# Kernel optimization log

Hardware: AMD Instinct MI355X
Metric: run time of the kernel (lower is better)

## Reference

```python
import jax, jax.numpy as jnp
import numpy as np

B, S, E, H = 4, 2048, 1024, 16
D = E // H  # head_dim = 64


def setup_inputs() -> dict:
    key = jax.random.key(0)
    ks = jax.random.split(key, 5)
    return {
        "x": jax.random.normal(ks[0], (B, S, E), dtype=jnp.float32),
        "w_qkv": jax.random.normal(ks[1], (3 * E, E), dtype=jnp.float32) * (E ** -0.5),
        "b_qkv": jax.random.normal(ks[2], (3 * E,), dtype=jnp.float32) * 0.02,
        "w_proj": jax.random.normal(ks[3], (E, E), dtype=jnp.float32) * (E ** -0.5),
        "b_proj": jax.random.normal(ks[4], (E,), dtype=jnp.float32) * 0.02,
    }


def reference(x, w_qkv, b_qkv, w_proj, b_proj):
    # fused QKV projection: [B,S,E] -> [B,S,3E] -> [B,S,3,H,D]
    qkv = (jnp.einsum("bse,fe->bsf", x, w_qkv) + b_qkv).reshape(B, S, 3, H, D)
    q, k, v = qkv[:, :, 0], qkv[:, :, 1], qkv[:, :, 2]  # each [B,S,H,D]
    scale = 1.0 / jnp.sqrt(jnp.asarray(D, dtype=q.dtype))
    scores = jnp.einsum("bqhd,bkhd->bhqk", q, k) * scale  # [B,H,S,S]
    attn = jax.nn.softmax(scores, axis=-1)
    out = jnp.einsum("bhqk,bkhd->bqhd", attn, v).reshape(B, S, E)
    return jnp.einsum("bse,fe->bsf", out, w_proj) + b_proj
```

## Files before the change

### kernel.cpp

```cpp
#include <hip/hip_runtime.h>
#include <cstdint>
#include <cstddef>

#define B_ 4
#define S_ 2048
#define E_ 1024
#define H_ 16
#define D_ 64
#define M_ (B_*S_)
#define NE_ ((size_t)B_*H_*S_*D_)

typedef unsigned int  u32;
typedef unsigned short u16;
typedef __attribute__((ext_vector_type(8))) short bf16x8;
typedef __attribute__((ext_vector_type(4))) float f32x4;
typedef __attribute__((ext_vector_type(2))) unsigned int u32x2;

__device__ __forceinline__ u16 f2bf(float x) {
    u32 u = __float_as_uint(x);
    u32 r = (u + 0x7FFFu + ((u >> 16) & 1u)) >> 16;
    return (u16)r;
}
__device__ __forceinline__ float bf2f(u16 h) { return __uint_as_float((u32)h << 16); }

__device__ __forceinline__ u32 cvtpk_bf16(float lo, float hi) {
    u32 r;
    asm("v_cvt_pk_bf16_f32 %0, %1, %2" : "=v"(r) : "v"(lo), "v"(hi));
    return r;
}

__device__ __forceinline__ void gload_lds16(const void* gsrc, void* lds) {
    __builtin_amdgcn_global_load_lds(
        (const __attribute__((address_space(1))) u32*)gsrc,
        (__attribute__((address_space(3))) u32*)lds, 16, 0, 0);
}


__global__ __launch_bounds__(256)
void convert_img(const float* __restrict__ src, u16* __restrict__ dh, u16* __restrict__ dl)
{
    const int tile = blockIdx.x;
    const int rt = tile >> 5, kt = tile & 31;
    const size_t tb = (size_t)tile * 2048;
    const int ci = threadIdx.x;
    const int l  = ci >> 3;
    const int ph = ci & 7;
    const int s  = ph ^ (l & 7);
    const int r  = (l << 1) | (s >> 2);
    const int k0 = (s & 3) << 3;
    const float* sp = src + ((size_t)(rt * 64 + r)) * 1024 + kt * 32 + k0;
    const float4 f0 = *(const float4*)sp;
    const float4 f1 = *(const float4*)(sp + 4);
    const float vals[8] = {f0.x, f0.y, f0.z, f0.w, f1.x, f1.y, f1.z, f1.w};
    __align__(16) short hs[8];
    __align__(16) short ls[8];
    #pragma unroll
    for (int j = 0; j < 8; ++j) {
        const u16 h = f2bf(vals[j]);
        hs[j] = (short)h;
        ls[j] = (short)f2bf(vals[j] - bf2f(h));
    }
    *(bf16x8*)(dh + tb + ci * 8) = *(const bf16x8*)hs;
    *(bf16x8*)(dl + tb + ci * 8) = *(const bf16x8*)ls;
}

template<int MODE>
__global__ __launch_bounds__(512, 2)
void gemm_mfma(const u16* __restrict__ AIh, const u16* __restrict__ AIl,
               const u16* __restrict__ BIh, const u16* __restrict__ BIl,
               const float* __restrict__ bias, float* __restrict__ Cout,
               u16* __restrict__ qh, u16* __restrict__ ql,
               u16* __restrict__ kh,
               u16* __restrict__ vh, u16* __restrict__ vl)
{
    __shared__ __align__(16) u16 sT[2][12][2048];

    const int tid = threadIdx.x, lane = tid & 63, w = tid >> 6;
    const int quad = lane >> 4, l15 = lane & 15;
    const int m0  = blockIdx.x * 256;
    const int n0  = blockIdx.y * 128;
    const int mt0 = blockIdx.x * 4;
    const int nt0 = blockIdx.y * 2;
    const int rw  = w >> 1;
    const int cw  = w & 1;

    const u16* srcq[6];
    #pragma unroll
    for (int it = 0; it < 6; ++it) {
        const int g = w * 6 + it;
        const int t = g >> 2, qtr = g & 3;
        const u16* img = (t < 4) ? AIh : (t < 8) ? AIl : (t < 10) ? BIh : BIl;
        const int rtile = (t < 8) ? (mt0 + (t & 3)) : (nt0 + (t & 1));
        srcq[it] = img + (size_t)rtile * (32 * 2048) + qtr * 512 + lane * 8;
    }

    f32x4 acc[4][4];
    #pragma unroll
    for (int i = 0; i < 4; ++i)
        #pragma unroll
        for (int j = 0; j < 4; ++j)
            acc[i][j] = (f32x4){0.f, 0.f, 0.f, 0.f};

    #pragma unroll
    for (int it = 0; it < 6; ++it)
        gload_lds16(srcq[it], (char*)&sT[0][0][0] + (w * 6 + it) * 1024);
    __syncthreads();

    #pragma unroll 2
    for (int kt = 0; kt < 32; ++kt) {
        const int cur = kt & 1;
        bf16x8 aH[4], aL[4], bH[4], bL[4];
        #pragma unroll
        for (int i = 0; i < 4; ++i) {
            const int r = i * 16 + l15, l = r >> 1;
            const int off = l * 64 + (((((r & 1) << 2) + quad) ^ (l & 7)) << 3);
            aH[i] = *(const bf16x8*)&sT[cur][rw][off];
            aL[i] = *(const bf16x8*)&sT[cur][4 + rw][off];
        }
        #pragma unroll
        for (int j = 0; j < 4; ++j) {
            const int r = j * 16 + l15, l = r >> 1;
            const int off = l * 64 + (((((r & 1) << 2) + quad) ^ (l & 7)) << 3);
            bH[j] = *(const bf16x8*)&sT[cur][8 + cw][off];
            bL[j] = *(const bf16x8*)&sT[cur][10 + cw][off];
        }
        if (kt < 31) {
            #pragma unroll
            for (int it = 0; it < 6; ++it)
                gload_lds16(srcq[it] + (size_t)(kt + 1) * 2048,
                            (char*)&sT[cur ^ 1][0][0] + (w * 6 + it) * 1024);
        }
        __builtin_amdgcn_s_setprio(1);
        #pragma unroll
        for (int i = 0; i < 4; ++i)
            #pragma unroll
            for (int j = 0; j < 4; ++j) {
                acc[i][j] = __builtin_amdgcn_mfma_f32_16x16x32_bf16(aL[i], bH[j], acc[i][j], 0, 0, 0);
                acc[i][j] = __builtin_amdgcn_mfma_f32_16x16x32_bf16(aH[i], bL[j], acc[i][j], 0, 0, 0);
                acc[i][j] = __builtin_amdgcn_mfma_f32_16x16x32_bf16(aH[i], bH[j], acc[i][j], 0, 0, 0);
            }
        __builtin_amdgcn_s_setprio(0);
        __syncthreads();
    }

    const int fbase = n0 + cw * 64;
    float bj[4];
    #pragma unroll
    for (int j = 0; j < 4; ++j) bj[j] = bias[fbase + j * 16 + l15];

    if (MODE == 0) {
        const int cR = fbase >> 10;
        const int hh = (fbase >> 6) & 15;
        #pragma unroll
        for (int i = 0; i < 4; ++i)
            #pragma unroll
            for (int j = 0; j < 4; ++j)
                #pragma unroll
                for (int reg = 0; reg < 4; ++reg) {
                    float val = acc[i][j][reg] + bj[j];
                    const int m = m0 + rw * 64 + i * 16 + quad * 4 + reg;
                    const int d = j * 16 + l15;
                    const int bb = m >> 11, s = m & 2047;
                    const int bh = bb * 16 + hh;
                    if (cR == 0) val *= 0.18033688011112042f;
                    const u16 h = f2bf(val);
                    if (cR == 0) {
                        const u16 lo = f2bf(val - bf2f(h));
                        const size_t idx = ((size_t)bh * 2048 + s) * 64 + d;
                        qh[idx] = h; ql[idx] = lo;
                    } else if (cR == 1) {
                        const size_t tile = (size_t)bh * 32 + (s >> 6);
                        const int r = s & 63;
                        const size_t off = (tile << 12) + r * 64 + (((d >> 3) ^ (r & 7)) << 3) + (d & 7);
                        kh[off] = h;
                    } else {
                        const u16 lo = f2bf(val - bf2f(h));
                        const size_t tile = (size_t)bh * 32 + (s >> 6);
                        const size_t off = (tile << 12) + d * 64 + ((((s & 63) >> 3) ^ (d & 7)) << 3) + (s & 7);
                        vh[off] = h; vl[off] = lo;
                    }
                }
    } else {
        #pragma unroll
        for (int i = 0; i < 4; ++i)
            #pragma unroll
            for (int j = 0; j < 4; ++j)
                #pragma unroll
                for (int reg = 0; reg < 4; ++reg) {
                    const int m = m0 + rw * 64 + i * 16 + quad * 4 + reg;
                    const int f = fbase + j * 16 + l15;
                    Cout[(size_t)m * 1024 + f] = acc[i][j][reg] + bj[j];
                }
    }
}

__global__ __launch_bounds__(256, 3)
void attn_mfma(const u16* __restrict__ qh, const u16* __restrict__ ql,
               const u16* __restrict__ kh,
               const u16* __restrict__ vh, const u16* __restrict__ vl,
               u16* __restrict__ oh, u16* __restrict__ ol)
{
    __shared__ __align__(16) u16 KV[3][4096];

    const int tid  = threadIdx.x;
    const int lane = tid & 63, w = tid >> 6;
    const int quad = lane >> 4, l15 = lane & 15;
    const int bh = blockIdx.y;
    const int q0 = blockIdx.x * 128 + w * 32;

    bf16x8 Qf[2][2][2];
    #pragma unroll
    for (int qs = 0; qs < 2; ++qs)
        #pragma unroll
        for (int kk = 0; kk < 2; ++kk) {
            const size_t idx = ((size_t)bh * S_ + q0 + qs * 16 + l15) * 64 + kk * 32 + quad * 8;
            Qf[qs][kk][0] = *(const bf16x8*)(qh + idx);
            Qf[qs][kk][1] = *(const bf16x8*)(ql + idx);
        }

    f32x4 O[2][4];
    float l_part[2] = {0.f, 0.f};
    #pragma unroll
    for (int qs = 0; qs < 2; ++qs)
        #pragma unroll
        for (int ds = 0; ds < 4; ++ds)
            O[qs][ds] = (f32x4){0.f, 0.f, 0.f, 0.f};

    const char* gk[3] = {(const char*)kh, (const char*)vh, (const char*)vl};

    for (int kt = 0; kt < S_ / 64; ++kt) {
        __syncthreads();
        const size_t tb = (((size_t)bh * 32 + kt) << 13);
        #pragma unroll
        for (int a = 0; a < 3; ++a)
            #pragma unroll
            for (int it = 0; it < 2; ++it) {
                const int off = w * 2048 + it * 1024;
                gload_lds16(gk[a] + tb + off + lane * 16, (char*)&KV[a][0] + off);
            }
        __syncthreads();

        f32x4 S[2][4];
        #pragma unroll
        for (int qs = 0; qs < 2; ++qs)
            #pragma unroll
            for (int ks = 0; ks < 4; ++ks)
                S[qs][ks] = (f32x4){-23.083120654223414f, -23.083120654223414f,
                                    -23.083120654223414f, -23.083120654223414f};

        __builtin_amdgcn_s_setprio(1);
        #pragma unroll
        for (int ks = 0; ks < 4; ++ks) {
            const int r = ks * 16 + l15;
            #pragma unroll
            for (int kk = 0; kk < 2; ++kk) {
                const int c = (kk * 4 + quad) ^ (r & 7);
                const bf16x8 Kh = *(const bf16x8*)&KV[0][r * 64 + c * 8];
                #pragma unroll
                for (int qs = 0; qs < 2; ++qs) {
                    S[qs][ks] = __builtin_amdgcn_mfma_f32_16x16x32_bf16(Kh, Qf[qs][kk][1], S[qs][ks], 0, 0, 0);
                    S[qs][ks] = __builtin_amdgcn_mfma_f32_16x16x32_bf16(Kh, Qf[qs][kk][0], S[qs][ks], 0, 0, 0);
                }
            }
        }
        __builtin_amdgcn_s_setprio(0);

        u32 PA[2][2][4];
        #pragma unroll
        for (int qs = 0; qs < 2; ++qs) {
            float lsum = 0.f;
            u32 PK[4][2];
            #pragma unroll
            for (int ks = 0; ks < 4; ++ks) {
                const float p0 = __builtin_exp2f(S[qs][ks][0]);
                const float p1 = __builtin_exp2f(S[qs][ks][1]);
                const float p2 = __builtin_exp2f(S[qs][ks][2]);
                const float p3 = __builtin_exp2f(S[qs][ks][3]);
                lsum += (p0 + p1) + (p2 + p3);
                PK[ks][0] = cvtpk_bf16(p0, p1);
                PK[ks][1] = cvtpk_bf16(p2, p3);
            }
            l_part[qs] += lsum;
            #pragma unroll
            for (int kk = 0; kk < 2; ++kk) {
                const u32x2 t0 = __builtin_amdgcn_permlane32_swap(PK[2 * kk][0], PK[2 * kk + 1][0], false, false);
                const u32x2 w02 = __builtin_amdgcn_permlane16_swap(t0.x, t0.y, false, false);
                const u32x2 t1 = __builtin_amdgcn_permlane32_swap(PK[2 * kk][1], PK[2 * kk + 1][1], false, false);
                const u32x2 w13 = __builtin_amdgcn_permlane16_swap(t1.x, t1.y, false, false);
                PA[qs][kk][0] = w02.x;
                PA[qs][kk][1] = w13.x;
                PA[qs][kk][2] = w02.y;
                PA[qs][kk][3] = w13.y;
            }
        }

        __builtin_amdgcn_s_setprio(1);
        #pragma unroll
        for (int kk = 0; kk < 2; ++kk) {
            union { u32 w4[4]; bf16x8 v; } pu0, pu1;
            #pragma unroll
            for (int c = 0; c < 4; ++c) { pu0.w4[c] = PA[0][kk][c]; pu1.w4[c] = PA[1][kk][c]; }
            const bf16x8 paf[2] = {pu0.v, pu1.v};
            #pragma unroll
            for (int ds = 0; ds < 4; ++ds) {
                const int r = ds * 16 + l15;
                const int c = (kk * 4 + quad) ^ (r & 7);
                const bf16x8 Vh = *(const bf16x8*)&KV[1][r * 64 + c * 8];
                const bf16x8 Vl = *(const bf16x8*)&KV[2][r * 64 + c * 8];
                #pragma unroll
                for (int qs = 0; qs < 2; ++qs) {
                    O[qs][ds] = __builtin_amdgcn_mfma_f32_16x16x32_bf16(Vl, paf[qs], O[qs][ds], 0, 0, 0);
                    O[qs][ds] = __builtin_amdgcn_mfma_f32_16x16x32_bf16(Vh, paf[qs], O[qs][ds], 0, 0, 0);
                }
            }
        }
        __builtin_amdgcn_s_setprio(0);
    }

    float linv[2];
    #pragma unroll
    for (int qs = 0; qs < 2; ++qs) {
        float rs = l_part[qs];
        rs += __shfl_xor(rs, 16);
        rs += __shfl_xor(rs, 32);
        linv[qs] = 1.f / rs;
    }

    const int bb = bh >> 4, hh = bh & 15;
    #pragma unroll
    for (int qs = 0; qs < 2; ++qs) {
        const float inv = linv[qs];
        const int s = q0 + qs * 16 + l15;
        const int m = bb * 2048 + s;
        const int mt = m >> 6, r = m & 63;
        const int l = r >> 1;
        const size_t tb0 = ((size_t)(mt * 32 + hh * 2)) * 2048;
        #pragma unroll
        for (int ds = 0; ds < 4; ++ds) {
            const int d0 = ds * 16 + quad * 4;
            const float v0 = O[qs][ds][0] * inv;
            const float v1 = O[qs][ds][1] * inv;
            const float v2 = O[qs][ds][2] * inv;
            const float v3 = O[qs][ds][3] * inv;
            const u32 h01 = cvtpk_bf16(v0, v1);
            const u32 h23 = cvtpk_bf16(v2, v3);
            const float r0 = v0 - bf2f((u16)h01);
            const float r1 = v1 - bf2f((u16)(h01 >> 16));
            const float r2 = v2 - bf2f((u16)h23);
            const float r3 = v3 - bf2f((u16)(h23 >> 16));
            const u32 l01 = cvtpk_bf16(r0, r1);
            const u32 l23 = cvtpk_bf16(r2, r3);
            const int c  = (d0 & 31) >> 3;
            const int ph = (((r & 1) << 2) + c) ^ (l & 7);
            const size_t off = tb0 + (size_t)(d0 >> 5) * 2048 + l * 64 + ph * 8 + (d0 & 7);
            *(u32x2*)(oh + off) = (u32x2){h01, h23};
            *(u32x2*)(ol + off) = (u32x2){l01, l23};
        }
    }
}

extern "C" void kernel_launch(void* const* d_in, const int* in_sizes, int n_in,
                              void* d_out, int out_size, void* d_ws, size_t ws_size,
                              hipStream_t stream) {
    const float* x      = (const float*)d_in[0];
    const float* w_qkv  = (const float*)d_in[1];
    const float* b_qkv  = (const float*)d_in[2];
    const float* w_proj = (const float*)d_in[3];
    const float* b_proj = (const float*)d_in[4];
    float* out = (float*)d_out;

    u16* qh  = (u16*)d_ws;
    u16* ql  = qh + NE_;
    u16* kh  = ql + NE_;
    u16* vh  = kh + NE_;
    u16* vl  = vh + NE_;
    u16* xh  = vl + NE_;
    u16* xl  = xh + NE_;
    u16* wqh = xl + NE_;
    u16* wql = wqh + (size_t)3 * 1024 * 1024;
    u16* oh  = xh;
    u16* ol  = xl;
    u16* wph = wqh;
    u16* wpl = wph + (size_t)1024 * 1024;

    convert_img<<<128 * 32, 256, 0, stream>>>(x, xh, xl);
    convert_img<<<48 * 32, 256, 0, stream>>>(w_qkv, wqh, wql);

    {
        dim3 grid(M_ / 256, (3 * E_) / 128);
        gemm_mfma<0><<<grid, 512, 0, stream>>>(xh, xl, wqh, wql,
                                               b_qkv, nullptr, qh, ql, kh, vh, vl);
    }
    {
        dim3 grid(S_ / 128, B_ * H_);
        attn_mfma<<<grid, 256, 0, stream>>>(qh, ql, kh, vh, vl, oh, ol);
    }
    convert_img<<<16 * 32, 256, 0, stream>>>(w_proj, wph, wpl);
    {
        dim3 grid(M_ / 256, E_ / 128);
        gemm_mfma<1><<<grid, 512, 0, stream>>>(oh, ol, wph, wpl,
                                               b_proj, out, nullptr, nullptr, nullptr,
                                               nullptr, nullptr);
    }
}
```

Measured before the change: 429.9 us.

## Triple-buffer GEMM LDS pipeline with vmcnt waits and XCD-aware block swizzle

The QKV and output-projection GEMM kernels move from a double-buffered LDS pipeline to a three-stage ring. Two k-tiles are prefetched ahead, and each iteration uses an explicit s_waitcnt vmcnt plus s_barrier instead of a trailing __syncthreads. The 2D grid becomes a 1D grid remapped so that consecutive blocks land on the same chiplet, aiming for better L2 reuse. LDS use rises to 144 KB and launch bounds drop to one block per CU, so occupancy falls in exchange for deeper latency hiding.

New measurement: 444.3 us. 1.03x slower.

```diff
diff --git a/kernel.cpp b/kernel.cpp
--- a/kernel.cpp
+++ b/kernel.cpp
@@ -65,7 +65,7 @@
 }
 
 template<int MODE>
-__global__ __launch_bounds__(512, 2)
+__global__ __launch_bounds__(512, 1)
 void gemm_mfma(const u16* __restrict__ AIh, const u16* __restrict__ AIl,
                const u16* __restrict__ BIh, const u16* __restrict__ BIl,
                const float* __restrict__ bias, float* __restrict__ Cout,
@@ -73,14 +73,22 @@
                u16* __restrict__ kh,
                u16* __restrict__ vh, u16* __restrict__ vl)
 {
-    __shared__ __align__(16) u16 sT[2][12][2048];
+    __shared__ __align__(16) u16 sT[3][12][2048];
+
+    constexpr int GY = (MODE == 0) ? 24 : 8;
+    constexpr int NCH = (32 * GY) >> 3;
 
     const int tid = threadIdx.x, lane = tid & 63, w = tid >> 6;
     const int quad = lane >> 4, l15 = lane & 15;
-    const int m0  = blockIdx.x * 256;
-    const int n0  = blockIdx.y * 128;
-    const int mt0 = blockIdx.x * 4;
-    const int nt0 = blockIdx.y * 2;
+
+    const int flat = blockIdx.x;
+    const int swz  = (flat & 7) * NCH + (flat >> 3);
+    const int bx   = swz / GY, by = swz % GY;
+
+    const int m0  = bx * 256;
+    const int n0  = by * 128;
+    const int mt0 = bx * 4;
+    const int nt0 = by * 2;
     const int rw  = w >> 1;
     const int cw  = w & 1;
 
@@ -104,32 +112,40 @@
     #pragma unroll
     for (int it = 0; it < 6; ++it)
         gload_lds16(srcq[it], (char*)&sT[0][0][0] + (w * 6 + it) * 1024);
-    __syncthreads();
-
-    #pragma unroll 2
+    #pragma unroll
+    for (int it = 0; it < 6; ++it)
+        gload_lds16(srcq[it] + 2048, (char*)&sT[1][0][0] + (w * 6 + it) * 1024);
+
+    int cb = 0;
     for (int kt = 0; kt < 32; ++kt) {
-        const int cur = kt & 1;
+        if (kt < 31) asm volatile("s_waitcnt vmcnt(6)" ::: "memory");
+        else         asm volatile("s_waitcnt vmcnt(0)" ::: "memory");
+        asm volatile("s_barrier" ::: "memory");
+
+        if (kt + 2 < 32) {
+            int nb = cb + 2; if (nb >= 3) nb -= 3;
+            #pragma unroll
+            for (int it = 0; it < 6; ++it)
+                gload_lds16(srcq[it] + (size_t)(kt + 2) * 2048,
+                            (char*)&sT[nb][0][0] + (w * 6 + it) * 1024);
+        }
+
         bf16x8 aH[4], aL[4], bH[4], bL[4];
         #pragma unroll
         for (int i = 0; i < 4; ++i) {
             const int r = i * 16 + l15, l = r >> 1;
             const int off = l * 64 + (((((r & 1) << 2) + quad) ^ (l & 7)) << 3);
-            aH[i] = *(const bf16x8*)&sT[cur][rw][off];
-            aL[i] = *(const bf16x8*)&sT[cur][4 + rw][off];
+            aH[i] = *(const bf16x8*)&sT[cb][rw][off];
+            aL[i] = *(const bf16x8*)&sT[cb][4 + rw][off];
         }
         #pragma unroll
         for (int j = 0; j < 4; ++j) {
             const int r = j * 16 + l15, l = r >> 1;
             const int off = l * 64 + (((((r & 1) << 2) + quad) ^ (l & 7)) << 3);
-            bH[j] = *(const bf16x8*)&sT[cur][8 + cw][off];
-            bL[j] = *(const bf16x8*)&sT[cur][10 + cw][off];
-        }
-        if (kt < 31) {
-            #pragma unroll
-            for (int it = 0; it < 6; ++it)
-                gload_lds16(srcq[it] + (size_t)(kt + 1) * 2048,
-                            (char*)&sT[cur ^ 1][0][0] + (w * 6 + it) * 1024);
-        }
+            bH[j] = *(const bf16x8*)&sT[cb][8 + cw][off];
+            bL[j] = *(const bf16x8*)&sT[cb][10 + cw][off];
+        }
+
         __builtin_amdgcn_s_setprio(1);
         #pragma unroll
         for (int i = 0; i < 4; ++i)
@@ -140,7 +156,8 @@
                 acc[i][j] = __builtin_amdgcn_mfma_f32_16x16x32_bf16(aH[i], bH[j], acc[i][j], 0, 0, 0);
             }
         __builtin_amdgcn_s_setprio(0);
-        __syncthreads();
+
+        cb += 1; if (cb >= 3) cb = 0;
     }
 
     const int fbase = n0 + cw * 64;
@@ -387,7 +404,7 @@
     convert_img<<<48 * 32, 256, 0, stream>>>(w_qkv, wqh, wql);
 
     {
-        dim3 grid(M_ / 256, (3 * E_) / 128);
+        dim3 grid(32 * 24);
         gemm_mfma<0><<<grid, 512, 0, stream>>>(xh, xl, wqh, wql,
                                                b_qkv, nullptr, qh, ql, kh, vh, vl);
     }
@@ -397,7 +414,7 @@
     }
     convert_img<<<16 * 32, 256, 0, stream>>>(w_proj, wph, wpl);
     {
-        dim3 grid(M_ / 256, E_ / 128);
+        dim3 grid(32 * 8);
         gemm_mfma<1><<<grid, 512, 0, stream>>>(oh, ol, wph, wpl,
                                                b_proj, out, nullptr, nullptr, nullptr,
                                                nullptr, nullptr);
```
